# Performance work log

Hardware: AMD Instinct MI355X
Metric: run time of the kernel (lower is better)

The kernel has to match this reference:

```python
import jax, jax.numpy as jnp
import numpy as np

N_POINTS = 4000000
RESOLUTION = 512
HASHMAP_SIZE = 1 << 19  # 2**log2_hashmap_size
N_FEATURES = 4
# Instant-NGP style spatial-hash primes
PRIME_X = np.uint32(1)
PRIME_Y = np.uint32(2654435761)
PRIME_Z = np.uint32(805459861)


def setup_inputs() -> dict:
    key = jax.random.key(0)
    k1, k2 = jax.random.split(key)
    inputs = jax.random.randint(k1, (N_POINTS, 3), 0, RESOLUTION, dtype=jnp.int32)
    embeddings = jax.random.normal(k2, (HASHMAP_SIZE, N_FEATURES), dtype=jnp.float32)
    return {"inputs": inputs, "embeddings": embeddings,
            "resolution": RESOLUTION, "hashmap_size": HASHMAP_SIZE}


def _hash_index(coords_u32, hashmap_size):
    # coords_u32: [N,3] uint32; XOR-of-products spatial hash, modulo table size
    h = (coords_u32[:, 0] * PRIME_X) ^ (coords_u32[:, 1] * PRIME_Y) ^ (coords_u32[:, 2] * PRIME_Z)
    return (h % np.uint32(hashmap_size)).astype(jnp.int32)


def reference(inputs, embeddings, resolution, hashmap_size):
    # cnt_np_embed forward (axis='xy'):
    #   gather binarized (STE sign) embeddings by spatial hash of 3D int coords,
    #   scatter-count +1/-1 occurrences into a [scale, scale, F, 2] plane grid,
    #   then normalize to per-cell fractions (Bernoulli probabilities).
    scale = resolution - 2
    idx = _hash_index(inputs.astype(jnp.uint32), hashmap_size)      # [N]
    emb = embeddings[idx]                                           # [N, F] irregular gather
    # STE_binary forward: clamp then sign -> {-1, +1}
    b = jnp.where(emb >= 0, 1.0, -1.0).astype(emb.dtype)            # [N, F]
    pos = (1.0 + b) * 0.5                                           # 1 where +1
    neg = (1.0 - b) * 0.5                                           # 1 where -1
    # project onto the xy plane; clip coords into the (resolution-2)^2 grid
    u = jnp.clip(inputs[:, 0], 0, scale - 1)
    v = jnp.clip(inputs[:, 1], 0, scale - 1)
    cell = (u * scale + v).astype(jnp.int32)                        # [N]
    num_cells = scale * scale
    pn_pos = jax.ops.segment_sum(pos, cell, num_segments=num_cells)  # [S*S, F]
    pn_neg = jax.ops.segment_sum(neg, cell, num_segments=num_cells)  # [S*S, F]
    pn = jnp.stack([pn_pos, pn_neg], axis=-1).reshape(scale, scale, -1, 2)
    pn_sum = jnp.sum(pn, axis=-1, keepdims=True) + 1e-6
    return pn / pn_sum
```

## Files before the change

kernel.cpp:

```cpp
#include <hip/hip_runtime.h>

#define SCALE   510
#define NCELLS  (SCALE * SCALE)
#define NF      4
#define PRIME_Y 2654435761u
#define PRIME_Z 805459861u

#define NGRP    32
#define NBLKA   512
#define CAPA    320
#define SEGASTR 321
#define PAT     1024
#define SIGBLKS 256

#define NBKT    256
#define NBLKB   512
#define SUBS    16
#define CAPB    72
#define PBT     1024
#define LROWB   258

#define PHT     1024
#define SPILLCAP 65536

#define GSEGA_BYTES  ((size_t)NBLKA * NGRP * CAPA * 4)
#define RECS_BYTES   ((size_t)NBLKB * NBKT * CAPB * 2)
#define CNTA_BYTES   ((size_t)NGRP * NBLKA * 2)
#define CNTG_BYTES   ((size_t)NBKT * NBLKB * 2)
#define SIGN_BYTES   ((size_t)262144)
#define HDR_BYTES    ((size_t)256)
#define SPILLA_BYTES ((size_t)SPILLCAP * 8)
#define SPILLB_BYTES ((size_t)SPILLCAP * 4)

__device__ __forceinline__ void split_point(
        int x, int y, int z,
        unsigned int* __restrict__ segA, unsigned int* __restrict__ rankA,
        unsigned int* __restrict__ spillcnt, unsigned long long* __restrict__ spillA,
        unsigned int hmask) {
    unsigned int h = (unsigned int)x
                   ^ ((unsigned int)y * PRIME_Y)
                   ^ ((unsigned int)z * PRIME_Z);
    unsigned int idx = h & hmask;
    unsigned int g   = idx >> 14;
    unsigned int hl  = idx & 0x3FFFu;
    unsigned int u = (unsigned int)min(max(x, 0), SCALE - 1);
    unsigned int v = (unsigned int)min(max(y, 0), SCALE - 1);
    unsigned int w = (hl << 18) | (u << 9) | v;
    unsigned int r = atomicAdd(&rankA[g], 1u);
    if (r < CAPA) {
        segA[g * SEGASTR + r] = w;
    } else {
        unsigned int rs = atomicAdd(spillcnt, 1u);
        if (rs < SPILLCAP)
            spillA[rs] = ((unsigned long long)g << 32) | w;
    }
}

__global__ __launch_bounds__(PAT)
void hashsplit_kernel(const int* __restrict__ inputs,
                      const float4* __restrict__ emb,
                      unsigned int* __restrict__ gsegA,
                      unsigned short* __restrict__ cntA,
                      unsigned char* __restrict__ signtab,
                      unsigned int* __restrict__ hdr,
                      unsigned long long* __restrict__ spillA,
                      int n, unsigned int hmask) {
    __shared__ unsigned int   segA[NGRP * SEGASTR];
    __shared__ unsigned int   rankA[NGRP];
    __shared__ unsigned short cwA[NGRP];
    const int t = threadIdx.x, b0 = blockIdx.x;

    if (b0 < SIGBLKS) {
        unsigned int i = (unsigned int)b0 * PAT + t;
        float4 e0 = emb[2 * i + 0];
        float4 e1 = emb[2 * i + 1];
        unsigned int bb = 0;
        if (e0.x >= 0.0f) bb |= 1u << 0;
        if (e0.y >= 0.0f) bb |= 1u << 1;
        if (e0.z >= 0.0f) bb |= 1u << 2;
        if (e0.w >= 0.0f) bb |= 1u << 3;
        if (e1.x >= 0.0f) bb |= 1u << 4;
        if (e1.y >= 0.0f) bb |= 1u << 5;
        if (e1.z >= 0.0f) bb |= 1u << 6;
        if (e1.w >= 0.0f) bb |= 1u << 7;
        signtab[i] = (unsigned char)bb;
        return;
    }
    const int b = b0 - SIGBLKS;

    if (t < NGRP) rankA[t] = 0;
    __syncthreads();

    const int nquad = n >> 2;
    const int qpb = (nquad + NBLKA - 1) / NBLKA;
    const int q0 = b * qpb;
    const int q1 = min(q0 + qpb, nquad);
    const int4* in4 = (const int4*)inputs;
    for (int q = q0 + t; q < q1; q += PAT) {
        int4 A = in4[3 * q + 0];
        int4 B = in4[3 * q + 1];
        int4 C = in4[3 * q + 2];
        split_point(A.x, A.y, A.z, segA, rankA, hdr, spillA, hmask);
        split_point(A.w, B.x, B.y, segA, rankA, hdr, spillA, hmask);
        split_point(B.z, B.w, C.x, segA, rankA, hdr, spillA, hmask);
        split_point(C.y, C.z, C.w, segA, rankA, hdr, spillA, hmask);
    }
    if (b == 0 && t == 0) {
        for (int p = nquad * 4; p < n; ++p)
            split_point(inputs[3 * p], inputs[3 * p + 1], inputs[3 * p + 2],
                        segA, rankA, hdr, spillA, hmask);
    }
    __syncthreads();

    if (t < NGRP) {
        unsigned int c = min(rankA[t], (unsigned int)CAPA);
        cntA[t * NBLKA + b] = (unsigned short)c;
        cwA[t] = (unsigned short)min((c + 15u) & ~15u, (unsigned int)CAPA);
    }
    __syncthreads();

    for (int j = t; j < NGRP * CAPA; j += PAT) {
        const int g = j / CAPA, r = j % CAPA;
        if (r < (int)cwA[g])
            gsegA[(size_t)b * NGRP * CAPA + j] = segA[g * SEGASTR + r];
    }
}

__device__ __forceinline__ void proc_rec(
        unsigned int w,
        const unsigned int* __restrict__ slice,
        unsigned short* __restrict__ segB, unsigned int* __restrict__ rankB,
        unsigned int* __restrict__ spillcntB, unsigned int* __restrict__ spillB) {
    unsigned int hl = w >> 18;
    unsigned int u  = (w >> 9) & 0x1FFu;
    unsigned int v  = w & 0x1FFu;
    unsigned int nib = (slice[hl >> 3] >> ((hl & 7u) * 4u)) & 0xFu;
    unsigned int bkt = u >> 1;
    unsigned int rec = ((u & 1u) << 13) | (v << 4) | nib;
    unsigned int r = atomicAdd(&rankB[bkt], 1u);
    if (r < CAPB) {
        segB[r * LROWB + bkt] = (unsigned short)rec;
    } else {
        unsigned int rs = atomicAdd(spillcntB, 1u);
        if (rs < SPILLCAP) spillB[rs] = (bkt << 16) | rec;
    }
}

__global__ __launch_bounds__(PBT)
void binlookup_kernel(const unsigned int* __restrict__ gsegA,
                      const unsigned short* __restrict__ cntA,
                      const unsigned int* __restrict__ sig32,
                      unsigned short* __restrict__ recs,
                      unsigned short* __restrict__ cntg,
                      const unsigned int* __restrict__ hdr,
                      const unsigned long long* __restrict__ spillA,
                      unsigned int* __restrict__ spillcntB,
                      unsigned int* __restrict__ spillB) {
    __shared__ unsigned int   slice[2048];
    __shared__ unsigned short segB[CAPB * LROWB];
    __shared__ unsigned int   rankB[NBKT];
    __shared__ unsigned short cA[32];
    __shared__ unsigned short wlim[NBKT];
    const int t = threadIdx.x, b = blockIdx.x;
    const int g = b / SUBS, k = b % SUBS;
    if (t < NBKT) rankB[t] = 0;
    if (t < 32)  cA[t] = cntA[g * NBLKA + k * 32 + t];
    for (int i = t; i < 2048; i += PBT) slice[i] = sig32[g * 2048 + i];
    __syncthreads();

    for (int j = t; j < 32 * CAPA; j += PBT) {
        const int s = j / CAPA, r = j % CAPA;
        if (r < (int)cA[s]) {
            unsigned int w = gsegA[((size_t)(k * 32 + s) * NGRP + g) * CAPA + r];
            proc_rec(w, slice, segB, rankB, spillcntB, spillB);
        }
    }
    if (k == 0) {
        unsigned int ns = min(hdr[0], (unsigned int)SPILLCAP);
        for (unsigned int i2 = t; i2 < ns; i2 += PBT) {
            unsigned long long e = spillA[i2];
            if ((unsigned int)(e >> 32) == (unsigned int)g)
                proc_rec((unsigned int)e, slice, segB, rankB, spillcntB, spillB);
        }
    }
    __syncthreads();

    if (t < NBKT) {
        unsigned int c = min(rankB[t], (unsigned int)CAPB);
        cntg[t * NBLKB + b] = (unsigned short)c;
        wlim[t] = (unsigned short)min(((c + 31u) >> 5) << 4,
                                      (unsigned int)(CAPB / 2));
    }
    __syncthreads();

    unsigned int* gout = (unsigned int*)(recs + (size_t)b * NBKT * CAPB);
    for (int j = t; j < NBKT * CAPB / 2; j += PBT) {
        const int bkt = j / (CAPB / 2);
        const int wi  = j % (CAPB / 2);
        if (wi < (int)wlim[bkt]) {
            const int r = wi * 2;
            unsigned int lo = segB[r * LROWB + bkt];
            unsigned int hi = segB[(r + 1) * LROWB + bkt];
            gout[j] = lo | (hi << 16);
        }
    }
}

__device__ __forceinline__ void hist_add(unsigned long long* hist,
                                         unsigned int rec) {
    unsigned int nib = rec & 0xFu;
    unsigned int v   = (rec >> 4) & 0x1FFu;
    unsigned int ul  = rec >> 13;
    unsigned long long add = 1ull
        | ((unsigned long long)(nib & 1u)        << 12)
        | ((unsigned long long)((nib >> 1) & 1u) << 24)
        | ((unsigned long long)((nib >> 2) & 1u) << 36)
        | ((unsigned long long)((nib >> 3) & 1u) << 48);
    atomicAdd(&hist[ul * SCALE + v], add);
}

__global__ __launch_bounds__(PHT)
void histnorm_kernel(const unsigned short* __restrict__ recs,
                     const unsigned short* __restrict__ cntg,
                     const unsigned int* __restrict__ hdr,
                     const unsigned int* __restrict__ spillB,
                     float* __restrict__ out) {
    __shared__ unsigned long long hist[2 * SCALE];
    __shared__ unsigned short cl[NBLKB];
    const int t = threadIdx.x, b = blockIdx.x;
    for (int i = t; i < 2 * SCALE; i += PHT) hist[i] = 0;
    if (t < NBLKB) cl[t] = cntg[b * NBLKB + t];
    __syncthreads();

    for (int j = t; j < NBLKB * CAPB / 2; j += PHT) {
        const int s  = j / (CAPB / 2);
        const int wi = j % (CAPB / 2);
        const int c  = cl[s];
        const int wl = min(((c + 31) >> 5) << 4, CAPB / 2);
        if (wi < wl) {
            const unsigned int* segp = (const unsigned int*)
                (recs + ((size_t)s * NBKT + b) * CAPB);
            unsigned int w = segp[wi];
            const int r0 = wi * 2;
            if (r0 < c)     hist_add(hist, w & 0xFFFFu);
            if (r0 + 1 < c) hist_add(hist, w >> 16);
        }
    }
    const unsigned int ns = min(hdr[1], (unsigned int)SPILLCAP);
    for (unsigned int i2 = t; i2 < ns; i2 += PHT) {
        unsigned int w = spillB[i2];
        if ((int)(w >> 16) == b) hist_add(hist, w & 0xFFFFu);
    }
    __syncthreads();

    const size_t outbase = (size_t)(2 * b) * SCALE * 8;
    for (int c = t; c < 2 * SCALE; c += PHT) {
        unsigned long long vv = hist[c];
        float cc = (float)(unsigned int)(vv & 0xFFFull);
        float p0 = (float)(unsigned int)((vv >> 12) & 0xFFFull);
        float p1 = (float)(unsigned int)((vv >> 24) & 0xFFFull);
        float p2 = (float)(unsigned int)((vv >> 36) & 0xFFFull);
        float p3 = (float)(unsigned int)((vv >> 48) & 0xFFFull);
        float inv = 1.0f / (cc + 1e-6f);
        float4 o0, o1;
        o0.x = p0 * inv; o0.y = (cc - p0) * inv;
        o0.z = p1 * inv; o0.w = (cc - p1) * inv;
        o1.x = p2 * inv; o1.y = (cc - p2) * inv;
        o1.z = p3 * inv; o1.w = (cc - p3) * inv;
        float4* op = (float4*)(out + outbase + (size_t)c * 8);
        op[0] = o0;
        op[1] = o1;
    }
}

__global__ void scatter_fb_kernel(const int* __restrict__ inputs,
                                  const float4* __restrict__ emb,
                                  unsigned long long* __restrict__ cnt,
                                  int n, unsigned int hmask) {
    int i = blockIdx.x * blockDim.x + threadIdx.x;
    if (i >= n) return;
    int x = inputs[3 * i], y = inputs[3 * i + 1], z = inputs[3 * i + 2];
    unsigned int h = (unsigned int)x ^ ((unsigned int)y * PRIME_Y)
                   ^ ((unsigned int)z * PRIME_Z);
    float4 e = emb[h & hmask];
    unsigned long long add = 1ull;
    if (e.x >= 0.0f) add |= 1ull << 12;
    if (e.y >= 0.0f) add |= 1ull << 24;
    if (e.z >= 0.0f) add |= 1ull << 36;
    if (e.w >= 0.0f) add |= 1ull << 48;
    int u = min(max(x, 0), SCALE - 1);
    int v = min(max(y, 0), SCALE - 1);
    atomicAdd(&cnt[u * SCALE + v], add);
}

__global__ void normalize_fb_kernel(const unsigned long long* __restrict__ cnt,
                                    float* __restrict__ out) {
    int i = blockIdx.x * blockDim.x + threadIdx.x;
    if (i >= NCELLS) return;
    unsigned long long v = cnt[i];
    float c  = (float)(unsigned int)(v & 0xFFFull);
    float p0 = (float)(unsigned int)((v >> 12) & 0xFFFull);
    float p1 = (float)(unsigned int)((v >> 24) & 0xFFFull);
    float p2 = (float)(unsigned int)((v >> 36) & 0xFFFull);
    float p3 = (float)(unsigned int)((v >> 48) & 0xFFFull);
    float inv = 1.0f / (c + 1e-6f);
    float4 o0, o1;
    o0.x = p0 * inv; o0.y = (c - p0) * inv;
    o0.z = p1 * inv; o0.w = (c - p1) * inv;
    o1.x = p2 * inv; o1.y = (c - p2) * inv;
    o1.z = p3 * inv; o1.w = (c - p3) * inv;
    float4* outv = (float4*)(out + (size_t)i * 8);
    outv[0] = o0; outv[1] = o1;
}

extern "C" void kernel_launch(void* const* d_in, const int* in_sizes, int n_in,
                              void* d_out, int out_size, void* d_ws, size_t ws_size,
                              hipStream_t stream) {
    const int*    inputs = (const int*)d_in[0];
    const float4* emb    = (const float4*)d_in[1];
    int n = in_sizes[0] / 3;
    unsigned int hsize = (unsigned int)(in_sizes[1] / NF);
    unsigned int hmask = hsize - 1;

    const size_t need = GSEGA_BYTES + RECS_BYTES + CNTA_BYTES + CNTG_BYTES
                      + SIGN_BYTES + HDR_BYTES + SPILLA_BYTES + SPILLB_BYTES;

    if (ws_size >= need && hsize == (1u << 19)) {
        char* w = (char*)d_ws;
        unsigned int*       gsegA   = (unsigned int*)w;            w += GSEGA_BYTES;
        unsigned short*     recs    = (unsigned short*)w;          w += RECS_BYTES;
        unsigned short*     cntA    = (unsigned short*)w;          w += CNTA_BYTES;
        unsigned short*     cntg    = (unsigned short*)w;          w += CNTG_BYTES;
        unsigned char*      signtab = (unsigned char*)w;           w += SIGN_BYTES;
        unsigned int*       hdr     = (unsigned int*)w;            w += HDR_BYTES;
        unsigned long long* spillA  = (unsigned long long*)w;      w += SPILLA_BYTES;
        unsigned int*       spillB  = (unsigned int*)w;

        hipMemsetAsync(hdr, 0, 8, stream);
        hashsplit_kernel<<<SIGBLKS + NBLKA, PAT, 0, stream>>>(
            inputs, emb, gsegA, cntA, signtab, hdr, spillA, n, hmask);
        binlookup_kernel<<<NBLKB, PBT, 0, stream>>>(
            gsegA, cntA, (const unsigned int*)signtab, recs, cntg,
            hdr, spillA, hdr + 1, spillB);
        histnorm_kernel<<<255, PHT, 0, stream>>>(
            recs, cntg, hdr, spillB, (float*)d_out);
    } else {
        unsigned long long* cnt = (unsigned long long*)d_ws;
        hipMemsetAsync(cnt, 0, (size_t)NCELLS * 8, stream);
        const int threads = 256;
        scatter_fb_kernel<<<(n + threads - 1) / threads, threads, 0, stream>>>(
            inputs, emb, cnt, n, hmask);
        normalize_fb_kernel<<<(NCELLS + threads - 1) / threads, threads, 0, stream>>>(
            cnt, (float*)d_out);
    }
}
```

Baseline: 47.84 us.

## Fuse hash-split, bin-lookup and histogram phases into one cooperative kernel

The three separate kernels become device functions that share one dynamic shared-memory buffer. They run inside a single cooperative mega-kernel of 512 blocks, separated by grid-wide syncs. The sign-table build is folded into the phase-A blocks instead of using 256 extra blocks. The aim is to remove inter-kernel launch gaps and tail effects. It depends on all 512 blocks of 1024 threads being co-resident, and adds grid-sync cost. A non-cooperative multi-kernel path is kept as a fallback.

```diff
diff --git a/kernel.cpp b/kernel.cpp
--- a/kernel.cpp
+++ b/kernel.cpp
@@ -1,4 +1,7 @@
 #include <hip/hip_runtime.h>
+#include <hip/hip_cooperative_groups.h>
+
+namespace cg = cooperative_groups;
 
 #define SCALE   510
 #define NCELLS  (SCALE * SCALE)
@@ -7,30 +10,52 @@
 #define PRIME_Z 805459861u
 
 #define NGRP    32
-#define NBLKA   512
+#define NBLK    512
 #define CAPA    320
 #define SEGASTR 321
-#define PAT     1024
-#define SIGBLKS 256
-
 #define NBKT    256
-#define NBLKB   512
 #define SUBS    16
 #define CAPB    72
-#define PBT     1024
 #define LROWB   258
-
-#define PHT     1024
+#define NT      1024
 #define SPILLCAP 65536
 
-#define GSEGA_BYTES  ((size_t)NBLKA * NGRP * CAPA * 4)
-#define RECS_BYTES   ((size_t)NBLKB * NBKT * CAPB * 2)
-#define CNTA_BYTES   ((size_t)NGRP * NBLKA * 2)
-#define CNTG_BYTES   ((size_t)NBKT * NBLKB * 2)
+#define A_SEG_OFF   0
+#define A_RANK_OFF  41088
+#define A_CW_OFF    41216
+#define B_SLICE_OFF 0
+#define B_SEGB_OFF  8192
+#define B_RANK_OFF  45344
+#define B_CA_OFF    46368
+#define B_WLIM_OFF  46432
+#define H_HIST_OFF  0
+#define H_CL_OFF    8160
+#define SMEM_BYTES  47104
+
+#define GSEGA_BYTES  ((size_t)NBLK * NGRP * CAPA * 4)
+#define RECS_BYTES   ((size_t)NBLK * NBKT * CAPB * 2)
+#define CNTA_BYTES   ((size_t)NGRP * NBLK * 2)
+#define CNTG_BYTES   ((size_t)NBKT * NBLK * 2)
 #define SIGN_BYTES   ((size_t)262144)
 #define HDR_BYTES    ((size_t)256)
 #define SPILLA_BYTES ((size_t)SPILLCAP * 8)
 #define SPILLB_BYTES ((size_t)SPILLCAP * 4)
+
+__device__ __forceinline__ unsigned char make_signbyte(
+        const float4* __restrict__ emb, unsigned int i) {
+    float4 e0 = emb[2 * i + 0];
+    float4 e1 = emb[2 * i + 1];
+    unsigned int bb = 0;
+    if (e0.x >= 0.0f) bb |= 1u << 0;
+    if (e0.y >= 0.0f) bb |= 1u << 1;
+    if (e0.z >= 0.0f) bb |= 1u << 2;
+    if (e0.w >= 0.0f) bb |= 1u << 3;
+    if (e1.x >= 0.0f) bb |= 1u << 4;
+    if (e1.y >= 0.0f) bb |= 1u << 5;
+    if (e1.z >= 0.0f) bb |= 1u << 6;
+    if (e1.w >= 0.0f) bb |= 1u << 7;
+    return (unsigned char)bb;
+}
 
 __device__ __forceinline__ void split_point(
         int x, int y, int z,
@@ -56,47 +81,24 @@
     }
 }
 
-__global__ __launch_bounds__(PAT)
-void hashsplit_kernel(const int* __restrict__ inputs,
-                      const float4* __restrict__ emb,
-                      unsigned int* __restrict__ gsegA,
-                      unsigned short* __restrict__ cntA,
-                      unsigned char* __restrict__ signtab,
-                      unsigned int* __restrict__ hdr,
-                      unsigned long long* __restrict__ spillA,
-                      int n, unsigned int hmask) {
-    __shared__ unsigned int   segA[NGRP * SEGASTR];
-    __shared__ unsigned int   rankA[NGRP];
-    __shared__ unsigned short cwA[NGRP];
-    const int t = threadIdx.x, b0 = blockIdx.x;
-
-    if (b0 < SIGBLKS) {
-        unsigned int i = (unsigned int)b0 * PAT + t;
-        float4 e0 = emb[2 * i + 0];
-        float4 e1 = emb[2 * i + 1];
-        unsigned int bb = 0;
-        if (e0.x >= 0.0f) bb |= 1u << 0;
-        if (e0.y >= 0.0f) bb |= 1u << 1;
-        if (e0.z >= 0.0f) bb |= 1u << 2;
-        if (e0.w >= 0.0f) bb |= 1u << 3;
-        if (e1.x >= 0.0f) bb |= 1u << 4;
-        if (e1.y >= 0.0f) bb |= 1u << 5;
-        if (e1.z >= 0.0f) bb |= 1u << 6;
-        if (e1.w >= 0.0f) bb |= 1u << 7;
-        signtab[i] = (unsigned char)bb;
-        return;
-    }
-    const int b = b0 - SIGBLKS;
-
+__device__ __forceinline__ void phaseA(
+        int b, int t, char* smem,
+        const int* __restrict__ inputs,
+        unsigned int* __restrict__ gsegA, unsigned short* __restrict__ cntA,
+        unsigned int* __restrict__ hdr, unsigned long long* __restrict__ spillA,
+        int n, unsigned int hmask) {
+    unsigned int*   segA  = (unsigned int*)(smem + A_SEG_OFF);
+    unsigned int*   rankA = (unsigned int*)(smem + A_RANK_OFF);
+    unsigned short* cwA   = (unsigned short*)(smem + A_CW_OFF);
     if (t < NGRP) rankA[t] = 0;
     __syncthreads();
 
     const int nquad = n >> 2;
-    const int qpb = (nquad + NBLKA - 1) / NBLKA;
+    const int qpb = (nquad + NBLK - 1) / NBLK;
     const int q0 = b * qpb;
     const int q1 = min(q0 + qpb, nquad);
     const int4* in4 = (const int4*)inputs;
-    for (int q = q0 + t; q < q1; q += PAT) {
+    for (int q = q0 + t; q < q1; q += NT) {
         int4 A = in4[3 * q + 0];
         int4 B = in4[3 * q + 1];
         int4 C = in4[3 * q + 2];
@@ -114,12 +116,12 @@
 
     if (t < NGRP) {
         unsigned int c = min(rankA[t], (unsigned int)CAPA);
-        cntA[t * NBLKA + b] = (unsigned short)c;
+        cntA[t * NBLK + b] = (unsigned short)c;
         cwA[t] = (unsigned short)min((c + 15u) & ~15u, (unsigned int)CAPA);
     }
     __syncthreads();
 
-    for (int j = t; j < NGRP * CAPA; j += PAT) {
+    for (int j = t; j < NGRP * CAPA; j += NT) {
         const int g = j / CAPA, r = j % CAPA;
         if (r < (int)cwA[g])
             gsegA[(size_t)b * NGRP * CAPA + j] = segA[g * SEGASTR + r];
@@ -127,8 +129,7 @@
 }
 
 __device__ __forceinline__ void proc_rec(
-        unsigned int w,
-        const unsigned int* __restrict__ slice,
+        unsigned int w, const unsigned int* __restrict__ slice,
         unsigned short* __restrict__ segB, unsigned int* __restrict__ rankB,
         unsigned int* __restrict__ spillcntB, unsigned int* __restrict__ spillB) {
     unsigned int hl = w >> 18;
@@ -146,29 +147,25 @@
     }
 }
 
-__global__ __launch_bounds__(PBT)
-void binlookup_kernel(const unsigned int* __restrict__ gsegA,
-                      const unsigned short* __restrict__ cntA,
-                      const unsigned int* __restrict__ sig32,
-                      unsigned short* __restrict__ recs,
-                      unsigned short* __restrict__ cntg,
-                      const unsigned int* __restrict__ hdr,
-                      const unsigned long long* __restrict__ spillA,
-                      unsigned int* __restrict__ spillcntB,
-                      unsigned int* __restrict__ spillB) {
-    __shared__ unsigned int   slice[2048];
-    __shared__ unsigned short segB[CAPB * LROWB];
-    __shared__ unsigned int   rankB[NBKT];
-    __shared__ unsigned short cA[32];
-    __shared__ unsigned short wlim[NBKT];
-    const int t = threadIdx.x, b = blockIdx.x;
+__device__ __forceinline__ void phaseB(
+        int b, int t, char* smem,
+        const unsigned int* __restrict__ gsegA, const unsigned short* __restrict__ cntA,
+        const unsigned int* __restrict__ sig32,
+        unsigned short* __restrict__ recs, unsigned short* __restrict__ cntg,
+        const unsigned int* __restrict__ hdr, const unsigned long long* __restrict__ spillA,
+        unsigned int* __restrict__ spillcntB, unsigned int* __restrict__ spillB) {
+    unsigned int*   slice = (unsigned int*)(smem + B_SLICE_OFF);
+    unsigned short* segB  = (unsigned short*)(smem + B_SEGB_OFF);
+    unsigned int*   rankB = (unsigned int*)(smem + B_RANK_OFF);
+    unsigned short* cA    = (unsigned short*)(smem + B_CA_OFF);
+    unsigned short* wlim  = (unsigned short*)(smem + B_WLIM_OFF);
     const int g = b / SUBS, k = b % SUBS;
     if (t < NBKT) rankB[t] = 0;
-    if (t < 32)  cA[t] = cntA[g * NBLKA + k * 32 + t];
-    for (int i = t; i < 2048; i += PBT) slice[i] = sig32[g * 2048 + i];
-    __syncthreads();
-
-    for (int j = t; j < 32 * CAPA; j += PBT) {
+    if (t < 32)  cA[t] = cntA[g * NBLK + k * 32 + t];
+    for (int i = t; i < 2048; i += NT) slice[i] = sig32[g * 2048 + i];
+    __syncthreads();
+
+    for (int j = t; j < 32 * CAPA; j += NT) {
         const int s = j / CAPA, r = j % CAPA;
         if (r < (int)cA[s]) {
             unsigned int w = gsegA[((size_t)(k * 32 + s) * NGRP + g) * CAPA + r];
@@ -177,7 +174,7 @@
     }
     if (k == 0) {
         unsigned int ns = min(hdr[0], (unsigned int)SPILLCAP);
-        for (unsigned int i2 = t; i2 < ns; i2 += PBT) {
+        for (unsigned int i2 = t; i2 < ns; i2 += NT) {
             unsigned long long e = spillA[i2];
             if ((unsigned int)(e >> 32) == (unsigned int)g)
                 proc_rec((unsigned int)e, slice, segB, rankB, spillcntB, spillB);
@@ -187,14 +184,14 @@
 
     if (t < NBKT) {
         unsigned int c = min(rankB[t], (unsigned int)CAPB);
-        cntg[t * NBLKB + b] = (unsigned short)c;
+        cntg[t * NBLK + b] = (unsigned short)c;
         wlim[t] = (unsigned short)min(((c + 31u) >> 5) << 4,
                                       (unsigned int)(CAPB / 2));
     }
     __syncthreads();
 
     unsigned int* gout = (unsigned int*)(recs + (size_t)b * NBKT * CAPB);
-    for (int j = t; j < NBKT * CAPB / 2; j += PBT) {
+    for (int j = t; j < NBKT * CAPB / 2; j += NT) {
         const int bkt = j / (CAPB / 2);
         const int wi  = j % (CAPB / 2);
         if (wi < (int)wlim[bkt]) {
@@ -219,20 +216,18 @@
     atomicAdd(&hist[ul * SCALE + v], add);
 }
 
-__global__ __launch_bounds__(PHT)
-void histnorm_kernel(const unsigned short* __restrict__ recs,
-                     const unsigned short* __restrict__ cntg,
-                     const unsigned int* __restrict__ hdr,
-                     const unsigned int* __restrict__ spillB,
-                     float* __restrict__ out) {
-    __shared__ unsigned long long hist[2 * SCALE];
-    __shared__ unsigned short cl[NBLKB];
-    const int t = threadIdx.x, b = blockIdx.x;
-    for (int i = t; i < 2 * SCALE; i += PHT) hist[i] = 0;
-    if (t < NBLKB) cl[t] = cntg[b * NBLKB + t];
-    __syncthreads();
-
-    for (int j = t; j < NBLKB * CAPB / 2; j += PHT) {
+__device__ __forceinline__ void phaseH(
+        int b, int t, char* smem,
+        const unsigned short* __restrict__ recs, const unsigned short* __restrict__ cntg,
+        const unsigned int* __restrict__ hdr, const unsigned int* __restrict__ spillB,
+        float* __restrict__ out) {
+    unsigned long long* hist = (unsigned long long*)(smem + H_HIST_OFF);
+    unsigned short*     cl   = (unsigned short*)(smem + H_CL_OFF);
+    for (int i = t; i < 2 * SCALE; i += NT) hist[i] = 0;
+    if (t < NBLK) cl[t] = cntg[b * NBLK + t];
+    __syncthreads();
+
+    for (int j = t; j < NBLK * CAPB / 2; j += NT) {
         const int s  = j / (CAPB / 2);
         const int wi = j % (CAPB / 2);
         const int c  = cl[s];
@@ -247,14 +242,14 @@
         }
     }
     const unsigned int ns = min(hdr[1], (unsigned int)SPILLCAP);
-    for (unsigned int i2 = t; i2 < ns; i2 += PHT) {
+    for (unsigned int i2 = t; i2 < ns; i2 += NT) {
         unsigned int w = spillB[i2];
         if ((int)(w >> 16) == b) hist_add(hist, w & 0xFFFFu);
     }
     __syncthreads();
 
     const size_t outbase = (size_t)(2 * b) * SCALE * 8;
-    for (int c = t; c < 2 * SCALE; c += PHT) {
+    for (int c = t; c < 2 * SCALE; c += NT) {
         unsigned long long vv = hist[c];
         float cc = (float)(unsigned int)(vv & 0xFFFull);
         float p0 = (float)(unsigned int)((vv >> 12) & 0xFFFull);
@@ -271,6 +266,70 @@
         op[0] = o0;
         op[1] = o1;
     }
+}
+
+__global__ __launch_bounds__(NT, 8)
+void mega_kernel(const int* __restrict__ inputs, const float4* __restrict__ emb,
+                 unsigned int* __restrict__ gsegA, unsigned short* __restrict__ cntA,
+                 unsigned char* __restrict__ signtab, unsigned int* __restrict__ hdr,
+                 unsigned long long* __restrict__ spillA, unsigned int* __restrict__ spillB,
+                 unsigned short* __restrict__ recs, unsigned short* __restrict__ cntg,
+                 float* __restrict__ out, int n, unsigned int hmask) {
+    __shared__ __align__(16) char smem[SMEM_BYTES];
+    const int t = threadIdx.x, b = blockIdx.x;
+
+    phaseA(b, t, smem, inputs, gsegA, cntA, hdr, spillA, n, hmask);
+    if (t < 512) {
+        unsigned int i = (unsigned int)b * 512u + (unsigned int)t;
+        signtab[i] = make_signbyte(emb, i);
+    }
+    cg::this_grid().sync();
+
+    phaseB(b, t, smem, gsegA, cntA, (const unsigned int*)signtab,
+           recs, cntg, hdr, spillA, hdr + 1, spillB);
+    cg::this_grid().sync();
+
+    if (b < 255)
+        phaseH(b, t, smem, recs, cntg, hdr, spillB, out);
+}
+
+__global__ __launch_bounds__(NT)
+void signtab_kernel(const float4* __restrict__ emb,
+                    unsigned char* __restrict__ signtab) {
+    unsigned int i = blockIdx.x * NT + threadIdx.x;
+    signtab[i] = make_signbyte(emb, i);
+}
+
+__global__ __launch_bounds__(NT)
+void phaseA_kernel(const int* __restrict__ inputs,
+                   unsigned int* __restrict__ gsegA, unsigned short* __restrict__ cntA,
+                   unsigned int* __restrict__ hdr, unsigned long long* __restrict__ spillA,
+                   int n, unsigned int hmask) {
+    __shared__ __align__(16) char smem[SMEM_BYTES];
+    phaseA(blockIdx.x, threadIdx.x, smem, inputs, gsegA, cntA, hdr, spillA, n, hmask);
+}
+
+__global__ __launch_bounds__(NT)
+void phaseB_kernel(const unsigned int* __restrict__ gsegA,
+                   const unsigned short* __restrict__ cntA,
+                   const unsigned int* __restrict__ sig32,
+                   unsigned short* __restrict__ recs, unsigned short* __restrict__ cntg,
+                   unsigned int* __restrict__ hdr,
+                   const unsigned long long* __restrict__ spillA,
+                   unsigned int* __restrict__ spillB) {
+    __shared__ __align__(16) char smem[SMEM_BYTES];
+    phaseB(blockIdx.x, threadIdx.x, smem, gsegA, cntA, sig32, recs, cntg,
+           hdr, spillA, hdr + 1, spillB);
+}
+
+__global__ __launch_bounds__(NT)
+void phaseH_kernel(const unsigned short* __restrict__ recs,
+                   const unsigned short* __restrict__ cntg,
+                   const unsigned int* __restrict__ hdr,
+                   const unsigned int* __restrict__ spillB,
+                   float* __restrict__ out) {
+    __shared__ __align__(16) char smem[SMEM_BYTES];
+    phaseH(blockIdx.x, threadIdx.x, smem, recs, cntg, hdr, spillB, out);
 }
 
 __global__ void scatter_fb_kernel(const int* __restrict__ inputs,
@@ -321,6 +380,7 @@
     int n = in_sizes[0] / 3;
     unsigned int hsize = (unsigned int)(in_sizes[1] / NF);
     unsigned int hmask = hsize - 1;
+    float* outp = (float*)d_out;
 
     const size_t need = GSEGA_BYTES + RECS_BYTES + CNTA_BYTES + CNTG_BYTES
                       + SIGN_BYTES + HDR_BYTES + SPILLA_BYTES + SPILLB_BYTES;
@@ -337,13 +397,25 @@
         unsigned int*       spillB  = (unsigned int*)w;
 
         hipMemsetAsync(hdr, 0, 8, stream);
-        hashsplit_kernel<<<SIGBLKS + NBLKA, PAT, 0, stream>>>(
-            inputs, emb, gsegA, cntA, signtab, hdr, spillA, n, hmask);
-        binlookup_kernel<<<NBLKB, PBT, 0, stream>>>(
-            gsegA, cntA, (const unsigned int*)signtab, recs, cntg,
-            hdr, spillA, hdr + 1, spillB);
-        histnorm_kernel<<<255, PHT, 0, stream>>>(
-            recs, cntg, hdr, spillB, (float*)d_out);
+
+        int dev = 0, coop = 0;
+        hipGetDevice(&dev);
+        hipDeviceGetAttribute(&coop, hipDeviceAttributeCooperativeLaunch, dev);
+        if (coop) {
+            void* kargs[] = {
+                (void*)&inputs, (void*)&emb, (void*)&gsegA, (void*)&cntA,
+                (void*)&signtab, (void*)&hdr, (void*)&spillA, (void*)&spillB,
+                (void*)&recs, (void*)&cntg, (void*)&outp, (void*)&n, (void*)&hmask };
+            hipLaunchCooperativeKernel((void*)mega_kernel, dim3(NBLK), dim3(NT),
+                                       kargs, 0, stream);
+        } else {
+            signtab_kernel<<<256, NT, 0, stream>>>(emb, signtab);
+            phaseA_kernel<<<NBLK, NT, 0, stream>>>(inputs, gsegA, cntA, hdr,
+                                                   spillA, n, hmask);
+            phaseB_kernel<<<NBLK, NT, 0, stream>>>(gsegA, cntA,
+                (const unsigned int*)signtab, recs, cntg, hdr, spillA, spillB);
+            phaseH_kernel<<<255, NT, 0, stream>>>(recs, cntg, hdr, spillB, outp);
+        }
     } else {
         unsigned long long* cnt = (unsigned long long*)d_ws;
         hipMemsetAsync(cnt, 0, (size_t)NCELLS * 8, stream);
@@ -351,6 +423,6 @@
         scatter_fb_kernel<<<(n + threads - 1) / threads, threads, 0, stream>>>(
             inputs, emb, cnt, n, hmask);
         normalize_fb_kernel<<<(NCELLS + threads - 1) / threads, threads, 0, stream>>>(
-            cnt, (float*)d_out);
-    }
-}
+            cnt, outp);
+    }
+}
```

After: 167.1 us. +249.4%, slower.
